# Kernel optimization log

Hardware: AMD Instinct MI355X
Metric: run time of the kernel (lower is better)

The kernel has to match this reference:

```python
import jax, jax.numpy as jnp
import numpy as np

B, S, D, H, DFF = 8, 1024, 1024, 16, 4096
HD = D // H
EPS_COS = 1e-8
EPS_LN = 1e-5


def setup_inputs() -> dict:
    key = jax.random.key(0)
    ks = jax.random.split(key, 12)
    inp = {
        "x": jax.random.normal(ks[0], (B, S, D), jnp.float32),
        "ln1_w": jnp.ones((D,), jnp.float32),
        "ln1_b": jnp.zeros((D,), jnp.float32),
        "in_proj_w": jax.random.normal(ks[1], (3 * D, D), jnp.float32) * 0.02,
        "in_proj_b": jnp.zeros((3 * D,), jnp.float32),
        "out_proj_w": jax.random.normal(ks[2], (D, D), jnp.float32) * 0.02,
        "out_proj_b": jnp.zeros((D,), jnp.float32),
        "ln2_w": jnp.ones((D,), jnp.float32),
        "ln2_b": jnp.zeros((D,), jnp.float32),
        "mu_weight": jax.random.uniform(ks[3], (DFF, D), jnp.float32, -1.0, 1.0) * (1.0 / np.sqrt(D)),
        "sigma_weight": jax.random.normal(ks[4], (DFF, D), jnp.float32) * 0.02,
        "gate_param": jnp.full((DFF,), 0.1, jnp.float32),
        "mu_bias": jnp.zeros((DFF,), jnp.float32),
        "ffn2_w": jax.random.normal(ks[5], (D, DFF), jnp.float32) * 0.02,
        "ffn2_b": jnp.zeros((D,), jnp.float32),
    }
    return inp


def _layernorm(x, w, b):
    mu = jnp.mean(x, axis=-1, keepdims=True)
    var = jnp.mean(jnp.square(x - mu), axis=-1, keepdims=True)
    return (x - mu) * jax.lax.rsqrt(var + EPS_LN) * w + b


def _mha_causal(h, in_proj_w, in_proj_b, out_proj_w, out_proj_b):
    # h: [B,S,D]; combined qkv projection as in torch nn.MultiheadAttention
    qkv = h @ in_proj_w.T + in_proj_b                      # [B,S,3D]
    q, k, v = jnp.split(qkv, 3, axis=-1)
    def heads(t):
        return t.reshape(B, S, H, HD).transpose(0, 2, 1, 3)  # [B,H,S,HD]
    q, k, v = heads(q), heads(k), heads(v)
    logits = jnp.einsum("bhqd,bhkd->bhqk", q, k) / jnp.sqrt(jnp.float32(HD))
    causal = jnp.tril(jnp.ones((S, S), bool))
    logits = jnp.where(causal, logits, jnp.float32(-jnp.inf))
    attn = jax.nn.softmax(logits, axis=-1)
    o = jnp.einsum("bhqk,bhkd->bhqd", attn, v)
    o = o.transpose(0, 2, 1, 3).reshape(B, S, D)
    return o @ out_proj_w.T + out_proj_b


def _moie_linear(xr, mu_weight, sigma_weight, gate_param, mu_bias):
    # xr: [N,D]. cosine similarity via GEMM + norm reductions (no (N,out,in) blowup)
    keys = mu_weight * jax.nn.softplus(sigma_weight)       # [DFF,D]
    dots = xr @ keys.T                                      # [N,DFF]
    xn = jnp.maximum(jnp.linalg.norm(xr, axis=-1, keepdims=True), EPS_COS)
    kn = jnp.maximum(jnp.linalg.norm(keys, axis=-1), EPS_COS)
    scores = dots / (xn * kn[None, :])                      # [N,DFF]
    weights = jax.nn.relu(scores - gate_param[None, :])
    comp = xr @ mu_weight.T + mu_bias                       # [N,DFF]
    masked = comp * weights
    return masked, scores


def reference(x, ln1_w, ln1_b, in_proj_w, in_proj_b, out_proj_w, out_proj_b,
              ln2_w, ln2_b, mu_weight, sigma_weight, gate_param, mu_bias,
              ffn2_w, ffn2_b):
    h = _layernorm(x, ln1_w, ln1_b)
    attn_out = _mha_causal(h, in_proj_w, in_proj_b, out_proj_w, out_proj_b)
    x = x + attn_out
    ffn_in = _layernorm(x, ln2_w, ln2_b)
    xr = ffn_in.reshape(-1, D)                              # [N,D]
    masked, scores = _moie_linear(xr, mu_weight, sigma_weight, gate_param, mu_bias)
    ffn1_out = masked.reshape(B, S, DFF)
    act = jax.nn.silu(ffn1_out)
    ffn2_out = act @ ffn2_w.T + ffn2_b
    x = x + ffn2_out
    return x, scores, masked
```

## Files before the change

kernel.cpp:

```cpp
#include <hip/hip_runtime.h>

typedef unsigned short u16;
typedef unsigned int u32;
typedef unsigned long long u64;
typedef __attribute__((ext_vector_type(8))) short short8;
typedef __attribute__((ext_vector_type(4))) float f32x4;

#define DEV static __device__ __forceinline__

DEV u16 f2b(float f) {
  union { float f; u32 u; } a; a.f = f;
  u32 r = a.u + 0x7fffu + ((a.u >> 16) & 1u);
  return (u16)(r >> 16);
}

DEV f32x4 mfma16(short8 a, short8 b, f32x4 c) {
  return __builtin_amdgcn_mfma_f32_16x16x32_bf16(a, b, c, 0, 0, 0);
}

DEV void async16(const void* g, void* l) {
  __builtin_amdgcn_global_load_lds(
      (const __attribute__((address_space(1))) u32*)g,
      (__attribute__((address_space(3))) u32*)l, 16, 0, 0);
}

__global__ __launch_bounds__(256) void f2bf4(const float* __restrict__ src,
                                             u16* __restrict__ dst, int n4) {
  const int stride = gridDim.x * 256;
  for (int i = blockIdx.x * 256 + threadIdx.x; i < n4; i += stride) {
    const f32x4 v = ((const f32x4*)src)[i];
    union { u64 q; u16 s[4]; } pk;
    pk.s[0] = f2b(v[0]); pk.s[1] = f2b(v[1]); pk.s[2] = f2b(v[2]); pk.s[3] = f2b(v[3]);
    ((u64*)dst)[i] = pk.q;
  }
}

__global__ __launch_bounds__(256) void prep_keys(
    const float* __restrict__ mu, const float* __restrict__ sg,
    u16* __restrict__ wcat, float* __restrict__ kn) {
  __shared__ float s1[4];
  const int row = blockIdx.x, tid = threadIdx.x, lane = tid & 63, wave = tid >> 6;
  const f32x4 m = *(const f32x4*)(mu + (size_t)row * 1024 + tid * 4);
  const f32x4 s = *(const f32x4*)(sg + (size_t)row * 1024 + tid * 4);
  float q = 0.f;
  union { u64 q; u16 s[4]; } pkk, pkm;
  #pragma unroll
  for (int j = 0; j < 4; ++j) {
    const float sp = (s[j] > 20.f) ? s[j] : log1pf(__expf(s[j]));
    const float k = m[j] * sp;
    q += k * k;
    pkk.s[j] = f2b(k);
    pkm.s[j] = f2b(m[j]);
  }
  *(u64*)(wcat + (size_t)row * 1024 + tid * 4) = pkk.q;
  *(u64*)(wcat + (size_t)(4096 + row) * 1024 + tid * 4) = pkm.q;
  #pragma unroll
  for (int d = 1; d < 64; d <<= 1) q += __shfl_xor(q, d);
  if (lane == 0) s1[wave] = q;
  __syncthreads();
  if (tid == 0) kn[row] = 1.0f / fmaxf(sqrtf(s1[0] + s1[1] + s1[2] + s1[3]), 1e-8f);
}

__global__ __launch_bounds__(256) void ln_kernel(
    const float* __restrict__ x, const float* __restrict__ w,
    const float* __restrict__ b, u16* __restrict__ y, float* __restrict__ xn) {
  __shared__ float s1[4], s2[4];
  const int row = blockIdx.x, tid = threadIdx.x, lane = tid & 63, wave = tid >> 6;
  const f32x4 xv = *(const f32x4*)(x + (size_t)row * 1024 + tid * 4);
  float s = xv[0] + xv[1] + xv[2] + xv[3];
  float q = xv[0]*xv[0] + xv[1]*xv[1] + xv[2]*xv[2] + xv[3]*xv[3];
  #pragma unroll
  for (int d = 1; d < 64; d <<= 1) { s += __shfl_xor(s, d); q += __shfl_xor(q, d); }
  if (lane == 0) { s1[wave] = s; s2[wave] = q; }
  __syncthreads();
  s = s1[0] + s1[1] + s1[2] + s1[3];
  q = s2[0] + s2[1] + s2[2] + s2[3];
  const float mean = s * (1.f / 1024.f);
  const float inv = rsqrtf(q * (1.f / 1024.f) - mean * mean + 1e-5f);
  const f32x4 wv = *(const f32x4*)(w + tid * 4);
  const f32x4 bv = *(const f32x4*)(b + tid * 4);
  float yv[4];
  union { u64 q; u16 s[4]; } pk;
  #pragma unroll
  for (int j = 0; j < 4; ++j) {
    yv[j] = (xv[j] - mean) * inv * wv[j] + bv[j];
    pk.s[j] = f2b(yv[j]);
  }
  *(u64*)(y + (size_t)row * 1024 + tid * 4) = pk.q;
  if (xn) {
    float qs = yv[0]*yv[0] + yv[1]*yv[1] + yv[2]*yv[2] + yv[3]*yv[3];
    #pragma unroll
    for (int d = 1; d < 64; d <<= 1) qs += __shfl_xor(qs, d);
    __syncthreads();
    if (lane == 0) s1[wave] = qs;
    __syncthreads();
    if (tid == 0) xn[row] = 1.0f / fmaxf(sqrtf(s1[0] + s1[1] + s1[2] + s1[3]), 1e-8f);
  }
}

template<int MODE>
__global__ __launch_bounds__(512, 4) void gemm_bt(
    const u16* __restrict__ A, const u16* __restrict__ W,
    int M, int N, int K,
    const float* __restrict__ aux0, const float* __restrict__ aux1,
    const float* __restrict__ aux2, const float* __restrict__ aux3,
    float* __restrict__ fo0, float* __restrict__ fo1,
    u16* __restrict__ bo0, u16* __restrict__ bo1, u16* __restrict__ bo2) {
  constexpr bool TWOB = (MODE == 2);
  constexpr int BN = TWOB ? 128 : 256;
  constexpr int STRIDE = 12288;
  __shared__ __align__(16) u16 lds[3 * STRIDE];

  const int tid = threadIdx.x;
  const int lane = tid & 63, wave = tid >> 6;
  const int x = lane & 15, g = lane >> 4, h = x >> 1;
  const int wm = wave >> 2;
  const int wn = TWOB ? ((wave >> 1) & 1) : (wave & 3);
  const int wh = TWOB ? (wave & 1) : 0;

  const int bid = (int)blockIdx.x;
  const int local = bid >> 3;
  const int by = (bid & 7) * 8 + (local & 7);
  const int bx = local >> 3;
  const int m0 = by * 128, n0 = bx * BN;

  const int rpl = tid >> 3, j0 = tid & 7;
  const int prow = rpl * 2 + (j0 & 1);
  const int pcol = (((j0 >> 1) ^ (rpl & 3)) & 3) * 8;
  const u16* srcA = A + (size_t)(m0 + prow) * K + pcol;
  const u16* srcB0 = W + (size_t)(n0 + prow) * K + pcol;
  const u16* srcB1 = TWOB ? (W + (size_t)(4096 + n0 + prow) * K + pcol)
                          : (W + (size_t)(n0 + 128 + prow) * K + pcol);
  const int dA = tid * 8, dB0 = 4096 + tid * 8, dB1 = 8192 + tid * 8;

  const int lane_off = h * 64 + (((2 * g + (x & 1)) ^ ((h & 3) << 1)) * 8);
  const int aoff = wm * 2048 + lane_off;
  const int boff = 4096 + wh * 4096 + wn * 2048 + lane_off;

  f32x4 acc[4][4];
  #pragma unroll
  for (int f = 0; f < 4; ++f)
    #pragma unroll
    for (int j = 0; j < 4; ++j) acc[f][j] = (f32x4){0.f, 0.f, 0.f, 0.f};

  const int NT = K >> 5;
  auto stage = [&](int t, int b) {
    u16* buf = lds + b * STRIDE;
    const size_t ko = (size_t)t * 32;
    async16(srcA + ko, buf + dA);
    async16(srcB0 + ko, buf + dB0);
    async16(srcB1 + ko, buf + dB1);
  };
  stage(0, 0);
  stage(1, 1);
  int br = 0, bs = 2;
  for (int t = 0; t < NT; ++t) {
    if (t < NT - 1)
      asm volatile("s_waitcnt vmcnt(3)\n\ts_barrier" ::: "memory");
    else
      asm volatile("s_waitcnt vmcnt(0)\n\ts_barrier" ::: "memory");
    const u16* bufr = lds + br * STRIDE;
    short8 bfr[4], af[4];
    #pragma unroll
    for (int j = 0; j < 4; ++j) bfr[j] = *(const short8*)(bufr + boff + j * 512);
    #pragma unroll
    for (int f = 0; f < 4; ++f) af[f] = *(const short8*)(bufr + aoff + f * 512);
    if (t + 2 < NT) stage(t + 2, bs);
    __builtin_amdgcn_s_setprio(1);
    #pragma unroll
    for (int f = 0; f < 4; ++f)
      #pragma unroll
      for (int j = 0; j < 4; ++j) acc[f][j] = mfma16(af[f], bfr[j], acc[f][j]);
    __builtin_amdgcn_s_setprio(0);
    br = (br == 2) ? 0 : br + 1;
    bs = (bs == 2) ? 0 : bs + 1;
  }

  if constexpr (MODE == 2) {
    float* fl = (float*)lds;
    float* pf = fl + (wm * 2 + wn) * 4160;
    __syncthreads();
    if (wh == 0) {
      #pragma unroll
      for (int f = 0; f < 4; ++f)
        #pragma unroll
        for (int j = 0; j < 4; ++j) {
          const int row = m0 + wm * 64 + f * 16 + g * 4;
          const int cm = n0 + wn * 64 + j * 16 + x;
          const float kni = aux1[cm];
          #pragma unroll
          for (int r = 0; r < 4; ++r) {
            const float s = acc[f][j][r] * aux0[row + r] * kni;
            pf[(f * 16 + g * 4 + r) * 65 + j * 16 + x] = s;
            fo0[(size_t)(row + r) * 4096 + cm] = s;
          }
        }
    }
    __syncthreads();
    if (wh == 1) {
      #pragma unroll
      for (int f = 0; f < 4; ++f)
        #pragma unroll
        for (int j = 0; j < 4; ++j) {
          const int row = m0 + wm * 64 + f * 16 + g * 4;
          const int cm = n0 + wn * 64 + j * 16 + x;
          const float gt = aux3[cm], mb = aux2[cm];
          #pragma unroll
          for (int r = 0; r < 4; ++r) {
            const float s = pf[(f * 16 + g * 4 + r) * 65 + j * 16 + x];
            const float comp = acc[f][j][r] + mb;
            const float mk = comp * fmaxf(s - gt, 0.f);
            fo1[(size_t)(row + r) * 4096 + cm] = mk;
            bo0[(size_t)(row + r) * 4096 + cm] = f2b(mk / (1.f + __expf(-mk)));
          }
        }
    }
    return;
  }

  const int col_base = n0 + wn * 64;
  const int row_base = m0 + wm * 64;
  #pragma unroll
  for (int f = 0; f < 4; ++f)
    #pragma unroll
    for (int j = 0; j < 4; ++j)
      #pragma unroll
      for (int r = 0; r < 4; ++r) {
        const int row = row_base + f * 16 + g * 4 + r;
        const int col = col_base + j * 16 + x;
        float v = acc[f][j][r];
        if constexpr (MODE == 0) {
          v += aux0[col];
          const int part = col >> 10, cc = col & 1023;
          const int hh = cc >> 6, dd = cc & 63;
          const size_t idx = ((size_t)((row >> 10) * 16 + hh) * 1024 + (row & 1023)) * 64 + dd;
          if (part == 0) bo0[idx] = f2b(v * 0.125f);
          else if (part == 1) bo1[idx] = f2b(v);
          else bo2[idx] = f2b(v);
        } else if constexpr (MODE == 1) {
          fo0[(size_t)row * 1024 + col] = v + aux0[col] + aux1[(size_t)row * 1024 + col];
        } else {
          fo0[(size_t)row * 1024 + col] = v + aux0[col] + aux1[(size_t)row * 1024 + col];
        }
      }
}

__global__ __launch_bounds__(256) void attn_kernel(
    const u16* __restrict__ Q, const u16* __restrict__ Kg,
    const u16* __restrict__ Vg, u16* __restrict__ O) {
  __shared__ __align__(16) u16 Kl[64 * 72];
  __shared__ __align__(16) u16 Vt[64 * 72];
  __shared__ __align__(16) u16 Pl[4][16 * 72];
  const int bh = blockIdx.x;
  const int qt = blockIdx.y;
  const int tid = threadIdx.x, lane = tid & 63, wave = tid >> 6;
  const int x = lane & 15, g = lane >> 4;
  const u16* Qb = Q + (size_t)bh * 1024 * 64;
  const u16* Kb = Kg + (size_t)bh * 1024 * 64;
  const u16* Vb = Vg + (size_t)bh * 1024 * 64;
  const int qbase = qt * 64 + wave * 16;
  const short8 qf0 = *(const short8*)&Qb[(qbase + x) * 64 + g * 8];
  const short8 qf1 = *(const short8*)&Qb[(qbase + x) * 64 + 32 + g * 8];
  float mrun[4], lrun[4];
  f32x4 oacc[4];
  #pragma unroll
  for (int r = 0; r < 4; ++r) { mrun[r] = -1e30f; lrun[r] = 0.f; }
  #pragma unroll
  for (int d = 0; d < 4; ++d) oacc[d] = (f32x4){0.f, 0.f, 0.f, 0.f};

  for (int t = 0; t <= qt; ++t) {
    __syncthreads();
    #pragma unroll
    for (int p = 0; p < 2; ++p) {
      const int s = tid + p * 256;
      const int row = s >> 3, c = s & 7;
      *(short8*)&Kl[row * 72 + c * 8] = *(const short8*)&Kb[(size_t)(t * 64 + row) * 64 + c * 8];
    }
    #pragma unroll
    for (int p = 0; p < 2; ++p) {
      const int kv = (tid >> 3) + p * 32;
      const int d0 = (tid & 7) * 8;
      const short8 v8 = *(const short8*)&Vb[(size_t)(t * 64 + kv) * 64 + d0];
      #pragma unroll
      for (int j = 0; j < 8; ++j) {
        const int d = d0 + j;
        Vt[d * 72 + ((kv + 8 * ((d >> 3) & 7)) & 63)] = (u16)v8[j];
      }
    }
    __syncthreads();

    float sc[4][4];
    #pragma unroll
    for (int nb = 0; nb < 4; ++nb) {
      f32x4 a = (f32x4){0.f, 0.f, 0.f, 0.f};
      const short8 kf0 = *(const short8*)&Kl[(nb * 16 + x) * 72 + g * 8];
      const short8 kf1 = *(const short8*)&Kl[(nb * 16 + x) * 72 + 32 + g * 8];
      a = mfma16(qf0, kf0, a);
      a = mfma16(qf1, kf1, a);
      #pragma unroll
      for (int r = 0; r < 4; ++r) sc[nb][r] = a[r];
    }
    if (t == qt) {
      #pragma unroll
      for (int nb = 0; nb < 4; ++nb)
        #pragma unroll
        for (int r = 0; r < 4; ++r)
          if (t * 64 + nb * 16 + x > qbase + g * 4 + r) sc[nb][r] = -1e30f;
    }
    float mnew[4], psum[4], scl[4];
    #pragma unroll
    for (int r = 0; r < 4; ++r) {
      float mx = fmaxf(fmaxf(sc[0][r], sc[1][r]), fmaxf(sc[2][r], sc[3][r]));
      #pragma unroll
      for (int d = 1; d < 16; d <<= 1) mx = fmaxf(mx, __shfl_xor(mx, d));
      mnew[r] = fmaxf(mrun[r], mx);
      scl[r] = __expf(mrun[r] - mnew[r]);
      mrun[r] = mnew[r];
      psum[r] = 0.f;
    }
    float p[4][4];
    #pragma unroll
    for (int nb = 0; nb < 4; ++nb)
      #pragma unroll
      for (int r = 0; r < 4; ++r) {
        p[nb][r] = __expf(sc[nb][r] - mnew[r]);
        psum[r] += p[nb][r];
      }
    #pragma unroll
    for (int r = 0; r < 4; ++r) {
      #pragma unroll
      for (int d = 1; d < 16; d <<= 1) psum[r] += __shfl_xor(psum[r], d);
      lrun[r] = lrun[r] * scl[r] + psum[r];
      #pragma unroll
      for (int db = 0; db < 4; ++db) oacc[db][r] *= scl[r];
    }
    u16* Pw = Pl[wave];
    #pragma unroll
    for (int nb = 0; nb < 4; ++nb)
      #pragma unroll
      for (int r = 0; r < 4; ++r)
        Pw[(g * 4 + r) * 72 + nb * 16 + x] = f2b(p[nb][r]);
    const short8 pf0 = *(const short8*)&Pw[x * 72 + g * 8];
    const short8 pf1 = *(const short8*)&Pw[x * 72 + 32 + g * 8];
    #pragma unroll
    for (int db = 0; db < 4; ++db) {
      const int d = db * 16 + x;
      const int swz = 8 * ((d >> 3) & 7);
      const short8 vf0 = *(const short8*)&Vt[d * 72 + ((g * 8 + swz) & 63)];
      const short8 vf1 = *(const short8*)&Vt[d * 72 + ((g * 8 + 32 + swz) & 63)];
      oacc[db] = mfma16(pf0, vf0, oacc[db]);
      oacc[db] = mfma16(pf1, vf1, oacc[db]);
    }
  }
  const int b = bh >> 4, hh = bh & 15;
  #pragma unroll
  for (int db = 0; db < 4; ++db)
    #pragma unroll
    for (int r = 0; r < 4; ++r) {
      const int qrow = qbase + g * 4 + r;
      O[((size_t)(b * 1024 + qrow)) * 1024 + hh * 64 + db * 16 + x] = f2b(oacc[db][r] / lrun[r]);
    }
}

extern "C" void kernel_launch(void* const* d_in, const int* in_sizes, int n_in,
                              void* d_out, int out_size, void* d_ws, size_t ws_size,
                              hipStream_t stream) {
  const float* x    = (const float*)d_in[0];
  const float* ln1w = (const float*)d_in[1];
  const float* ln1b = (const float*)d_in[2];
  const float* wip  = (const float*)d_in[3];
  const float* bip  = (const float*)d_in[4];
  const float* wop  = (const float*)d_in[5];
  const float* bop  = (const float*)d_in[6];
  const float* ln2w = (const float*)d_in[7];
  const float* ln2b = (const float*)d_in[8];
  const float* muw  = (const float*)d_in[9];
  const float* sgw  = (const float*)d_in[10];
  const float* gate = (const float*)d_in[11];
  const float* mub  = (const float*)d_in[12];
  const float* wf2  = (const float*)d_in[13];
  const float* bf2  = (const float*)d_in[14];

  float* out_x = (float*)d_out;
  float* out_scores = out_x + (size_t)8192 * 1024;
  float* out_masked = out_scores + (size_t)8192 * 4096;

  char* ws = (char*)d_ws;
  size_t off = 0;
  auto alloc = [&](size_t n) { char* p = ws + off; off += (n + 255) & ~(size_t)255; return p; };
  u16* h_bf    = (u16*)alloc((size_t)8192 * 1024 * 2);
  u16* q_bf    = (u16*)alloc((size_t)8192 * 1024 * 2);
  u16* k_bf    = (u16*)alloc((size_t)8192 * 1024 * 2);
  u16* v_bf    = (u16*)alloc((size_t)8192 * 1024 * 2);
  u16* o_bf    = (u16*)alloc((size_t)8192 * 1024 * 2);
  float* x_res = (float*)alloc((size_t)8192 * 1024 * 4);
  u16* xr_bf   = (u16*)alloc((size_t)8192 * 1024 * 2);
  float* xn    = (float*)alloc((size_t)8192 * 4);
  float* kn    = (float*)alloc((size_t)4096 * 4);
  u16* wcat    = (u16*)alloc((size_t)8192 * 1024 * 2);
  u16* wip_b   = (u16*)alloc((size_t)3072 * 1024 * 2);
  u16* wop_b   = (u16*)alloc((size_t)1024 * 1024 * 2);
  u16* wf2_b   = (u16*)alloc((size_t)1024 * 4096 * 2);
  u16* act_bf  = (u16*)alloc((size_t)8192 * 4096 * 2);

  f2bf4<<<1024, 256, 0, stream>>>(wip, wip_b, 3072 * 1024 / 4);
  f2bf4<<<512, 256, 0, stream>>>(wop, wop_b, 1024 * 1024 / 4);
  f2bf4<<<1024, 256, 0, stream>>>(wf2, wf2_b, 1024 * 4096 / 4);
  prep_keys<<<4096, 256, 0, stream>>>(muw, sgw, wcat, kn);
  ln_kernel<<<8192, 256, 0, stream>>>(x, ln1w, ln1b, h_bf, nullptr);
  gemm_bt<0><<<768, 512, 0, stream>>>(h_bf, wip_b, 8192, 3072, 1024,
      bip, nullptr, nullptr, nullptr, nullptr, nullptr, q_bf, k_bf, v_bf);
  attn_kernel<<<dim3(128, 16), 256, 0, stream>>>(q_bf, k_bf, v_bf, o_bf);
  gemm_bt<1><<<256, 512, 0, stream>>>(o_bf, wop_b, 8192, 1024, 1024,
      bop, x, nullptr, nullptr, x_res, nullptr, nullptr, nullptr, nullptr);
  ln_kernel<<<8192, 256, 0, stream>>>(x_res, ln2w, ln2b, xr_bf, xn);
  gemm_bt<2><<<2048, 512, 0, stream>>>(xr_bf, wcat, 8192, 4096, 1024,
      xn, kn, mub, gate, out_scores, out_masked, act_bf, nullptr, nullptr);
  gemm_bt<3><<<256, 512, 0, stream>>>(act_bf, wf2_b, 8192, 1024, 4096,
      bf2, x_res, nullptr, nullptr, out_x, nullptr, nullptr, nullptr, nullptr);
}
```

Baseline: 546.4 us.

## Switch GEMM to 4-wave blocks with 128-row per-wave tiles

Changes the shared GEMM kernel from 8 waves of 512 threads to 4 waves of 256 threads. Each wave now covers all 128 rows and a 64-column strip, so it holds 8x4 accumulator fragments instead of 4x4, and each thread issues six async loads per stage instead of three. The block swizzle becomes a generic grid-based mapping. This raises MFMA work per LDS fragment read and reduces barrier participants, at the cost of more registers per thread and lower occupancy, with fewer waves available to hide latency.

Measured after the change: 655.9 us. +20.0%, slower.

```diff
diff --git a/kernel.cpp b/kernel.cpp
--- a/kernel.cpp
+++ b/kernel.cpp
@@ -99,7 +99,7 @@
 }
 
 template<int MODE>
-__global__ __launch_bounds__(512, 4) void gemm_bt(
+__global__ __launch_bounds__(256, 2) void gemm_bt(
     const u16* __restrict__ A, const u16* __restrict__ W,
     int M, int N, int K,
     const float* __restrict__ aux0, const float* __restrict__ aux1,
@@ -107,39 +107,41 @@
     float* __restrict__ fo0, float* __restrict__ fo1,
     u16* __restrict__ bo0, u16* __restrict__ bo1, u16* __restrict__ bo2) {
   constexpr bool TWOB = (MODE == 2);
-  constexpr int BN = TWOB ? 128 : 256;
   constexpr int STRIDE = 12288;
   __shared__ __align__(16) u16 lds[3 * STRIDE];
 
   const int tid = threadIdx.x;
   const int lane = tid & 63, wave = tid >> 6;
   const int x = lane & 15, g = lane >> 4, h = x >> 1;
-  const int wm = wave >> 2;
-  const int wn = TWOB ? ((wave >> 1) & 1) : (wave & 3);
-  const int wh = TWOB ? (wave & 1) : 0;
+  const int wn = wave;
 
   const int bid = (int)blockIdx.x;
-  const int local = bid >> 3;
-  const int by = (bid & 7) * 8 + (local & 7);
-  const int bx = local >> 3;
-  const int m0 = by * 128, n0 = bx * BN;
+  const int gx = TWOB ? (N >> 7) : (N >> 8);
+  const int wg = (bid & 7) * ((int)gridDim.x >> 3) + (bid >> 3);
+  const int by = wg / gx, bx = wg - by * gx;
+  const int m0 = by * 128, n0 = bx * (TWOB ? 128 : 256);
 
   const int rpl = tid >> 3, j0 = tid & 7;
   const int prow = rpl * 2 + (j0 & 1);
   const int pcol = (((j0 >> 1) ^ (rpl & 3)) & 3) * 8;
-  const u16* srcA = A + (size_t)(m0 + prow) * K + pcol;
-  const u16* srcB0 = W + (size_t)(n0 + prow) * K + pcol;
-  const u16* srcB1 = TWOB ? (W + (size_t)(4096 + n0 + prow) * K + pcol)
-                          : (W + (size_t)(n0 + 128 + prow) * K + pcol);
-  const int dA = tid * 8, dB0 = 4096 + tid * 8, dB1 = 8192 + tid * 8;
+  const u16* srcA0 = A + (size_t)(m0 + prow) * K + pcol;
+  const u16* srcA1 = A + (size_t)(m0 + 64 + prow) * K + pcol;
+  const u16* srcB[4];
+  #pragma unroll
+  for (int i = 0; i < 4; ++i) {
+    if (TWOB)
+      srcB[i] = (i < 2) ? (W + (size_t)(n0 + i * 64 + prow) * K + pcol)
+                        : (W + (size_t)(4096 + n0 + (i - 2) * 64 + prow) * K + pcol);
+    else
+      srcB[i] = W + (size_t)(n0 + i * 64 + prow) * K + pcol;
+  }
 
   const int lane_off = h * 64 + (((2 * g + (x & 1)) ^ ((h & 3) << 1)) * 8);
-  const int aoff = wm * 2048 + lane_off;
-  const int boff = 4096 + wh * 4096 + wn * 2048 + lane_off;
-
-  f32x4 acc[4][4];
-  #pragma unroll
-  for (int f = 0; f < 4; ++f)
+  const int boff = 4096 + wn * 2048 + lane_off;
+
+  f32x4 acc[8][4];
+  #pragma unroll
+  for (int f = 0; f < 8; ++f)
     #pragma unroll
     for (int j = 0; j < 4; ++j) acc[f][j] = (f32x4){0.f, 0.f, 0.f, 0.f};
 
@@ -147,28 +149,29 @@
   auto stage = [&](int t, int b) {
     u16* buf = lds + b * STRIDE;
     const size_t ko = (size_t)t * 32;
-    async16(srcA + ko, buf + dA);
-    async16(srcB0 + ko, buf + dB0);
-    async16(srcB1 + ko, buf + dB1);
+    async16(srcA0 + ko, buf + tid * 8);
+    async16(srcA1 + ko, buf + 2048 + tid * 8);
+    #pragma unroll
+    for (int i = 0; i < 4; ++i) async16(srcB[i] + ko, buf + 4096 + i * 2048 + tid * 8);
   };
   stage(0, 0);
   stage(1, 1);
   int br = 0, bs = 2;
   for (int t = 0; t < NT; ++t) {
     if (t < NT - 1)
-      asm volatile("s_waitcnt vmcnt(3)\n\ts_barrier" ::: "memory");
+      asm volatile("s_waitcnt vmcnt(6)\n\ts_barrier" ::: "memory");
     else
       asm volatile("s_waitcnt vmcnt(0)\n\ts_barrier" ::: "memory");
     const u16* bufr = lds + br * STRIDE;
-    short8 bfr[4], af[4];
+    short8 bfr[4], af[8];
     #pragma unroll
     for (int j = 0; j < 4; ++j) bfr[j] = *(const short8*)(bufr + boff + j * 512);
     #pragma unroll
-    for (int f = 0; f < 4; ++f) af[f] = *(const short8*)(bufr + aoff + f * 512);
+    for (int f = 0; f < 8; ++f) af[f] = *(const short8*)(bufr + lane_off + f * 512);
     if (t + 2 < NT) stage(t + 2, bs);
     __builtin_amdgcn_s_setprio(1);
     #pragma unroll
-    for (int f = 0; f < 4; ++f)
+    for (int f = 0; f < 8; ++f)
       #pragma unroll
       for (int j = 0; j < 4; ++j) acc[f][j] = mfma16(af[f], bfr[j], acc[f][j]);
     __builtin_amdgcn_s_setprio(0);
@@ -178,14 +181,14 @@
 
   if constexpr (MODE == 2) {
     float* fl = (float*)lds;
-    float* pf = fl + (wm * 2 + wn) * 4160;
-    __syncthreads();
-    if (wh == 0) {
-      #pragma unroll
-      for (int f = 0; f < 4; ++f)
+    __syncthreads();
+    if (wn < 2) {
+      float* pf = fl + wn * 8320;
+      #pragma unroll
+      for (int f = 0; f < 8; ++f)
         #pragma unroll
         for (int j = 0; j < 4; ++j) {
-          const int row = m0 + wm * 64 + f * 16 + g * 4;
+          const int row = m0 + f * 16 + g * 4;
           const int cm = n0 + wn * 64 + j * 16 + x;
           const float kni = aux1[cm];
           #pragma unroll
@@ -197,13 +200,14 @@
         }
     }
     __syncthreads();
-    if (wh == 1) {
-      #pragma unroll
-      for (int f = 0; f < 4; ++f)
+    if (wn >= 2) {
+      float* pf = fl + (wn - 2) * 8320;
+      #pragma unroll
+      for (int f = 0; f < 8; ++f)
         #pragma unroll
         for (int j = 0; j < 4; ++j) {
-          const int row = m0 + wm * 64 + f * 16 + g * 4;
-          const int cm = n0 + wn * 64 + j * 16 + x;
+          const int row = m0 + f * 16 + g * 4;
+          const int cm = n0 + (wn - 2) * 64 + j * 16 + x;
           const float gt = aux3[cm], mb = aux2[cm];
           #pragma unroll
           for (int r = 0; r < 4; ++r) {
@@ -218,16 +222,14 @@
     return;
   }
 
-  const int col_base = n0 + wn * 64;
-  const int row_base = m0 + wm * 64;
-  #pragma unroll
-  for (int f = 0; f < 4; ++f)
+  #pragma unroll
+  for (int f = 0; f < 8; ++f)
     #pragma unroll
     for (int j = 0; j < 4; ++j)
       #pragma unroll
       for (int r = 0; r < 4; ++r) {
-        const int row = row_base + f * 16 + g * 4 + r;
-        const int col = col_base + j * 16 + x;
+        const int row = m0 + f * 16 + g * 4 + r;
+        const int col = n0 + wn * 64 + j * 16 + x;
         float v = acc[f][j][r];
         if constexpr (MODE == 0) {
           v += aux0[col];
@@ -237,8 +239,6 @@
           if (part == 0) bo0[idx] = f2b(v * 0.125f);
           else if (part == 1) bo1[idx] = f2b(v);
           else bo2[idx] = f2b(v);
-        } else if constexpr (MODE == 1) {
-          fo0[(size_t)row * 1024 + col] = v + aux0[col] + aux1[(size_t)row * 1024 + col];
         } else {
           fo0[(size_t)row * 1024 + col] = v + aux0[col] + aux1[(size_t)row * 1024 + col];
         }
@@ -408,14 +408,14 @@
   f2bf4<<<1024, 256, 0, stream>>>(wf2, wf2_b, 1024 * 4096 / 4);
   prep_keys<<<4096, 256, 0, stream>>>(muw, sgw, wcat, kn);
   ln_kernel<<<8192, 256, 0, stream>>>(x, ln1w, ln1b, h_bf, nullptr);
-  gemm_bt<0><<<768, 512, 0, stream>>>(h_bf, wip_b, 8192, 3072, 1024,
+  gemm_bt<0><<<768, 256, 0, stream>>>(h_bf, wip_b, 8192, 3072, 1024,
       bip, nullptr, nullptr, nullptr, nullptr, nullptr, q_bf, k_bf, v_bf);
   attn_kernel<<<dim3(128, 16), 256, 0, stream>>>(q_bf, k_bf, v_bf, o_bf);
-  gemm_bt<1><<<256, 512, 0, stream>>>(o_bf, wop_b, 8192, 1024, 1024,
+  gemm_bt<1><<<256, 256, 0, stream>>>(o_bf, wop_b, 8192, 1024, 1024,
       bop, x, nullptr, nullptr, x_res, nullptr, nullptr, nullptr, nullptr);
   ln_kernel<<<8192, 256, 0, stream>>>(x_res, ln2w, ln2b, xr_bf, xn);
-  gemm_bt<2><<<2048, 512, 0, stream>>>(xr_bf, wcat, 8192, 4096, 1024,
+  gemm_bt<2><<<2048, 256, 0, stream>>>(xr_bf, wcat, 8192, 4096, 1024,
       xn, kn, mub, gate, out_scores, out_masked, act_bf, nullptr, nullptr);
-  gemm_bt<3><<<256, 512, 0, stream>>>(act_bf, wf2_b, 8192, 1024, 4096,
+  gemm_bt<3><<<256, 256, 0, stream>>>(act_bf, wf2_b, 8192, 1024, 4096,
       bf2, x_res, nullptr, nullptr, out_x, nullptr, nullptr, nullptr, nullptr);
 }
```
